# Kernel optimization log

Measured on AMD Instinct MI355X. Metric: run time of the kernel, lower is better.

The kernel has to match this reference:

```python
import jax, jax.numpy as jnp
import numpy as np

EPS = 1e-5  # BatchNorm eps (torch default)
PAD = 1
K = 9  # 3x3 kernel points

def conv3x3(x, w, b):
    # x: [B,C,H,W], w: [O,C,3,3]
    y = jax.lax.conv_general_dilated(x, w, (1, 1), ((PAD, PAD), (PAD, PAD)),
                                     dimension_numbers=('NCHW', 'OIHW', 'NCHW'))
    return y + b[None, :, None, None]

def deform_conv2d(x, offset, mask, weight, bias):
    # Modulated deformable conv v2, stride 1, pad 1, 3x3 kernel.
    # x: [B,C,H,W]; offset: [B,2K,H,W] (first K = dy, last K = dx); mask: [B,K,H,W]
    B, C, H, W = x.shape
    ki, kj = jnp.meshgrid(jnp.arange(3), jnp.arange(3), indexing='ij')
    ki = ki.reshape(K).astype(x.dtype)
    kj = kj.reshape(K).astype(x.dtype)
    dy = offset[:, :K].transpose(0, 2, 3, 1)   # [B,H,W,K]
    dx = offset[:, K:].transpose(0, 2, 3, 1)
    m = mask.transpose(0, 2, 3, 1)             # [B,H,W,K]
    hs = jnp.arange(H, dtype=x.dtype)
    ws = jnp.arange(W, dtype=x.dtype)
    py = hs[None, :, None, None] - PAD + ki[None, None, None, :] + dy  # [B,H,W,K]
    px = ws[None, None, :, None] - PAD + kj[None, None, None, :] + dx
    y0 = jnp.floor(py)
    x0 = jnp.floor(px)
    wy1 = py - y0
    wx1 = px - x0
    wy0 = 1.0 - wy1
    wx0 = 1.0 - wx1

    def gather(yi, xi):
        valid = ((yi >= 0) & (yi < H) & (xi >= 0) & (xi < W)).astype(x.dtype)
        yc = jnp.clip(yi, 0, H - 1).astype(jnp.int32)
        xc = jnp.clip(xi, 0, W - 1).astype(jnp.int32)
        g = jax.vmap(lambda img, yb, xb: img[:, yb, xb])(x, yc, xc)  # [B,C,H,W,K]
        return g * valid[:, None]

    val = (gather(y0, x0) * (wy0 * wx0)[:, None]
           + gather(y0, x0 + 1.0) * (wy0 * wx1)[:, None]
           + gather(y0 + 1.0, x0) * (wy1 * wx0)[:, None]
           + gather(y0 + 1.0, x0 + 1.0) * (wy1 * wx1)[:, None])
    val = val * m[:, None]  # modulation
    out = jnp.einsum('bchwk,ock->bohw', val, weight.reshape(weight.shape[0], C, K))
    return out + bias[None, :, None, None]

def dcnv2(x, w_om, b_om, w, b, gamma, beta, mean, var):
    om = conv3x3(x, w_om, b_om)               # [B,27,H,W]
    o1, o2, mr = jnp.split(om, 3, axis=1)
    offset = jnp.concatenate([o1, o2], axis=1)  # [B,18,H,W]
    mask = jax.nn.sigmoid(mr)
    y = deform_conv2d(x, offset, mask, w, b)
    scale = (gamma / jnp.sqrt(var + EPS))[None, :, None, None]
    y = (y - mean[None, :, None, None]) * scale + beta[None, :, None, None]
    return jax.nn.silu(y)

def setup_inputs() -> dict:
    key = jax.random.key(0)
    ks = jax.random.split(key, 9)
    B, C, H, W = 4, 256, 128, 128
    C4 = C // 4
    return {
        'x': jax.random.normal(ks[0], (B, C, H, W), jnp.float32),
        'w': jax.random.normal(ks[1], (4, C4, C4, 3, 3), jnp.float32) * 0.05,
        'b': jax.random.normal(ks[2], (4, C4), jnp.float32) * 0.05,
        'w_om': jax.random.normal(ks[3], (4, 27, C4, 3, 3), jnp.float32) * 0.01,
        'b_om': jax.random.normal(ks[4], (4, 27), jnp.float32) * 0.01,
        'gamma': jax.random.normal(ks[5], (4, C4), jnp.float32) * 0.1 + 1.0,
        'beta': jax.random.normal(ks[6], (4, C4), jnp.float32) * 0.1,
        'mean': jax.random.normal(ks[7], (4, C4), jnp.float32) * 0.1,
        'var': jax.random.uniform(ks[8], (4, C4), jnp.float32, minval=0.5, maxval=1.5),
    }

def reference(x, w, b, w_om, b_om, gamma, beta, mean, var):
    B, C, H, W = x.shape
    C4 = C // 4
    # channel-split into 4 independent groups, vmap identical DCNv2 over groups
    xg = x.reshape(B, 4, C4, H, W).transpose(1, 0, 2, 3, 4)  # [4,B,C4,H,W]
    yg = jax.vmap(dcnv2)(xg, w_om, b_om, w, b, gamma, beta, mean, var)
    return yg.transpose(1, 0, 2, 3, 4).reshape(B, C, H, W)
```

## Files before the change

### kernel.cpp

```cpp
#include <hip/hip_runtime.h>
#include <math.h>

#define Hs 128
#define Ws 128
#define HWs 16384

typedef __attribute__((ext_vector_type(8))) short short8;
typedef __attribute__((ext_vector_type(8))) __bf16 bf16x8;
typedef __attribute__((ext_vector_type(4))) float f32x4;

static __device__ __forceinline__ float bf2f(unsigned short u) {
    union { unsigned int i; float f; } v; v.i = ((unsigned int)u) << 16; return v.f;
}
static __device__ __forceinline__ unsigned short f2bf(float f) {
    unsigned int u = __builtin_bit_cast(unsigned int, f);
    return (unsigned short)((u + 0x7fffu + ((u >> 16) & 1u)) >> 16);
}
static __device__ __forceinline__ unsigned int pack2bf(float a0, float a1) {
    return (unsigned int)f2bf(a0) | ((unsigned int)f2bf(a1) << 16);
}
static __device__ __forceinline__ f32x4 mfma16(short8 a, short8 b, f32x4 c) {
    return __builtin_amdgcn_mfma_f32_16x16x32_bf16(
        __builtin_bit_cast(bf16x8, a), __builtin_bit_cast(bf16x8, b), c, 0, 0, 0);
}

__global__ void k_prep(const float* __restrict__ w, const float* __restrict__ b,
                       const float* __restrict__ w_om,
                       const float* __restrict__ gamma, const float* __restrict__ beta,
                       const float* __restrict__ mean, const float* __restrict__ var,
                       unsigned short* __restrict__ w2, unsigned short* __restrict__ wom2,
                       float* __restrict__ scsh) {
    int idx = blockIdx.x * 256 + threadIdx.x;
    if (idx < 4 * 64 * 576) {
        int go = idx / 576;
        int ck = idx - go * 576;
        int k = ck >> 6, c = ck & 63;
        w2[idx] = f2bf(w[go * 576 + c * 9 + k]);
    }
    if (idx < 4 * 32 * 576) {
        int gj = idx / 576;
        int g = gj >> 5, j = gj & 31;
        int ck = idx - gj * 576;
        int k = ck >> 6, c = ck & 63;
        float v = (j < 27) ? w_om[(g * 27 + j) * 576 + c * 9 + k] : 0.f;
        wom2[idx] = f2bf(v);
    }
    if (idx < 256) {
        float sc = gamma[idx] * rsqrtf(var[idx] + 1e-5f);
        scsh[idx] = sc;
        scsh[256 + idx] = (b[idx] - mean[idx]) * sc + beta[idx];
    }
}

__global__ __launch_bounds__(256) void k_xt(const float* __restrict__ x,
                                            unsigned short* __restrict__ xT) {
    const int img = blockIdx.y;
    const int g = img >> 2, bb = img & 3;
    const int p0 = blockIdx.x * 64;
    const int tid = threadIdx.x;
    __shared__ float t[64 * 65];

    const float* xg = x + (size_t)(bb * 256 + g * 64) * HWs + p0;
    const int pr = tid & 63, cw = tid >> 6;
#pragma unroll
    for (int i = 0; i < 16; ++i) {
        int c = i * 4 + cw;
        t[c * 65 + pr] = xg[(size_t)c * HWs + pr];
    }
    __syncthreads();
    const int p = tid >> 2, c16 = (tid & 3) * 16;
    unsigned short* dst = xT + (size_t)img * HWs * 64 + (size_t)(p0 + p) * 64 + c16;
    unsigned int rr[8];
#pragma unroll
    for (int q = 0; q < 8; ++q)
        rr[q] = pack2bf(t[(c16 + 2 * q) * 65 + p], t[(c16 + 2 * q + 1) * 65 + p]);
    *(uint4*)dst       = make_uint4(rr[0], rr[1], rr[2], rr[3]);
    *(uint4*)(dst + 8) = make_uint4(rr[4], rr[5], rr[6], rr[7]);
}

__global__ __launch_bounds__(256, 2) void k_off(const unsigned short* __restrict__ xT,
                                                const unsigned short* __restrict__ wom2,
                                                const float* __restrict__ b_om,
                                                float* __restrict__ om) {
    const int img = blockIdx.y;
    const int g = img >> 2;
    const int h = blockIdx.x;
    const int tid = threadIdx.x;
    const int lane = tid & 63, wv = tid >> 6;
    const int mt = wv & 1, nh = wv >> 1;
    const int m = lane & 15, q = lane >> 4;

    __shared__ unsigned short xrow[3 * 130 * 72];

    const unsigned short* xTi = xT + (size_t)img * HWs * 64;
    for (int i = tid; i < 3 * 130 * 8; i += 256) {
        int rr = i / 1040;
        int rem = i - rr * 1040;
        int px = rem >> 3, j = rem & 7;
        int gh = h + rr - 1, gw = px - 1;
        uint4 v = make_uint4(0, 0, 0, 0);
        if (gh >= 0 && gh < Hs && gw >= 0 && gw < Ws)
            v = *(const uint4*)(xTi + (size_t)(gh * Ws + gw) * 64 + j * 8);
        *(uint4*)&xrow[(rr * 130 + px) * 72 + j * 8] = v;
    }

    short8 afrag[18];
    const unsigned short* wb = wom2 + (size_t)(g * 32 + mt * 16 + m) * 576 + q * 8;
#pragma unroll
    for (int t = 0; t < 18; ++t) afrag[t] = *(const short8*)(wb + t * 32);

    f32x4 acc[4];
#pragma unroll
    for (int t = 0; t < 4; ++t) acc[t] = (f32x4){0.f, 0.f, 0.f, 0.f};

    __syncthreads();

#pragma unroll
    for (int k = 0; k < 9; ++k) {
        const int ki = k / 3, kj = k - ki * 3;
#pragma unroll
        for (int s = 0; s < 2; ++s) {
#pragma unroll
            for (int t = 0; t < 4; ++t) {
                int px = (nh * 4 + t) * 16 + m + kj;
                short8 bfrag = *(const short8*)&xrow[(ki * 130 + px) * 72 + (s * 4 + q) * 8];
                acc[t] = mfma16(afrag[k * 2 + s], bfrag, acc[t]);
            }
        }
    }

    float* omi = om + (size_t)img * 27 * HWs + h * Ws;
#pragma unroll
    for (int t = 0; t < 4; ++t) {
#pragma unroll
        for (int r = 0; r < 4; ++r) {
            int j = mt * 16 + q * 4 + r;
            if (j < 27) {
                float v = acc[t][r] + b_om[g * 27 + j];
                if (j >= 18) v = 1.f / (1.f + __expf(-v));
                omi[(size_t)j * HWs + (nh * 4 + t) * 16 + m] = v;
            }
        }
    }
}

__global__ __launch_bounds__(256, 3) void k_def(const unsigned short* __restrict__ xT,
                                                const float* __restrict__ om,
                                                const unsigned short* __restrict__ w2,
                                                const float* __restrict__ scsh,
                                                float* __restrict__ out) {
    const int img = blockIdx.y;
    const int g = img >> 2, bb = img & 3;
    const int p0 = blockIdx.x * 64;
    const int tid = threadIdx.x;
    const int lane = tid & 63, wv = tid >> 6;
    const int m = lane & 15, q = lane >> 4;

    __shared__ int   pO[4][576];
    __shared__ float pW[4][576];
    __shared__ unsigned short val[64 * 72];
    __shared__ float lsc[64], lsh[64];

    if (tid < 64) {
        lsc[tid] = scsh[g * 64 + tid];
        lsh[tid] = scsh[256 + g * 64 + tid];
    }

    const float* omg = om + (size_t)img * 27 * HWs;
    for (int idx = tid; idx < 576; idx += 256) {
        int k = idx >> 6, pp = idx & 63;
        int p = p0 + pp;
        int h = p >> 7, w = p & 127;
        float dy = omg[k * HWs + p];
        float dx = omg[(9 + k) * HWs + p];
        float mk = omg[(18 + k) * HWs + p];
        int ki = k / 3, kj = k - ki * 3;
        float py = (float)(h - 1 + ki) + dy;
        float px = (float)(w - 1 + kj) + dx;
        float fy = floorf(py), fx = floorf(px);
        float wy1 = py - fy, wx1 = px - fx;
        float wy0 = 1.f - wy1, wx0 = 1.f - wx1;
        int y0 = (int)fy, x0 = (int)fx, y1 = y0 + 1, x1 = x0 + 1;
        bool vy0 = (y0 >= 0) && (y0 < Hs), vy1 = (y1 >= 0) && (y1 < Hs);
        bool vx0 = (x0 >= 0) && (x0 < Ws), vx1 = (x1 >= 0) && (x1 < Ws);
        int cy0 = min(max(y0, 0), Hs - 1), cy1 = min(max(y1, 0), Hs - 1);
        int cx0 = min(max(x0, 0), Ws - 1), cx1 = min(max(x1, 0), Ws - 1);
        pO[0][idx] = cy0 * Ws + cx0;
        pO[1][idx] = cy0 * Ws + cx1;
        pO[2][idx] = cy1 * Ws + cx0;
        pO[3][idx] = cy1 * Ws + cx1;
        pW[0][idx] = (vy0 && vx0) ? wy0 * wx0 * mk : 0.f;
        pW[1][idx] = (vy0 && vx1) ? wy0 * wx1 * mk : 0.f;
        pW[2][idx] = (vy1 && vx0) ? wy1 * wx0 * mk : 0.f;
        pW[3][idx] = (vy1 && vx1) ? wy1 * wx1 * mk : 0.f;
    }

    short8 afrag[18];
    const unsigned short* wb = w2 + (size_t)(g * 64 + wv * 16 + m) * 576 + q * 8;
#pragma unroll
    for (int t = 0; t < 18; ++t) afrag[t] = *(const short8*)(wb + t * 32);

    f32x4 acc[4];
#pragma unroll
    for (int t = 0; t < 4; ++t) acc[t] = (f32x4){0.f, 0.f, 0.f, 0.f};

    const unsigned short* xTi = xT + (size_t)img * HWs * 64;
    const int p = tid >> 2, c4 = tid & 3;

#pragma unroll
    for (int k = 0; k < 9; ++k) {
        __syncthreads();
        const int kb = k * 64 + p;
        const int off0 = pO[0][kb], off1 = pO[1][kb], off2 = pO[2][kb], off3 = pO[3][kb];
        const float w0f = pW[0][kb], w1f = pW[1][kb], w2f = pW[2][kb], w3f = pW[3][kb];
        const unsigned short* s0 = xTi + (size_t)off0 * 64;
        const unsigned short* s1 = xTi + (size_t)off1 * 64;
        const unsigned short* s2 = xTi + (size_t)off2 * 64;
        const unsigned short* s3 = xTi + (size_t)off3 * 64;
#pragma unroll
        for (int it = 0; it < 2; ++it) {
            const int oc8 = (c4 + it * 4) * 8;
            short8 x0v = *(const short8*)(s0 + oc8);
            short8 x1v = *(const short8*)(s1 + oc8);
            short8 x2v = *(const short8*)(s2 + oc8);
            short8 x3v = *(const short8*)(s3 + oc8);
            unsigned int rr[4];
#pragma unroll
            for (int e = 0; e < 4; ++e) {
                float a0 = w0f * bf2f((unsigned short)x0v[2 * e])
                         + w1f * bf2f((unsigned short)x1v[2 * e])
                         + w2f * bf2f((unsigned short)x2v[2 * e])
                         + w3f * bf2f((unsigned short)x3v[2 * e]);
                float a1 = w0f * bf2f((unsigned short)x0v[2 * e + 1])
                         + w1f * bf2f((unsigned short)x1v[2 * e + 1])
                         + w2f * bf2f((unsigned short)x2v[2 * e + 1])
                         + w3f * bf2f((unsigned short)x3v[2 * e + 1]);
                rr[e] = pack2bf(a0, a1);
            }
            *(uint4*)&val[p * 72 + oc8] = make_uint4(rr[0], rr[1], rr[2], rr[3]);
        }
        __syncthreads();
#pragma unroll
        for (int s = 0; s < 2; ++s) {
#pragma unroll
            for (int t = 0; t < 4; ++t) {
                short8 bfrag = *(const short8*)&val[(t * 16 + m) * 72 + s * 32 + q * 8];
                acc[t] = mfma16(afrag[k * 2 + s], bfrag, acc[t]);
            }
        }
    }

    float* outg = out + ((size_t)bb * 256 + g * 64) * HWs + p0;
#pragma unroll
    for (int t = 0; t < 4; ++t) {
#pragma unroll
        for (int r = 0; r < 4; ++r) {
            int o = wv * 16 + q * 4 + r;
            float y = acc[t][r] * lsc[o] + lsh[o];
            outg[(size_t)o * HWs + t * 16 + m] = y / (1.f + __expf(-y));
        }
    }
}

extern "C" void kernel_launch(void* const* d_in, const int* in_sizes, int n_in,
                              void* d_out, int out_size, void* d_ws, size_t ws_size,
                              hipStream_t stream) {
    const float* x     = (const float*)d_in[0];
    const float* w     = (const float*)d_in[1];
    const float* b     = (const float*)d_in[2];
    const float* w_om  = (const float*)d_in[3];
    const float* b_om  = (const float*)d_in[4];
    const float* gamma = (const float*)d_in[5];
    const float* beta  = (const float*)d_in[6];
    const float* mean  = (const float*)d_in[7];
    const float* var   = (const float*)d_in[8];
    float* out = (float*)d_out;

    char* ws = (char*)d_ws;
    float* om            = (float*)ws;
    unsigned short* xT   = (unsigned short*)(ws + 28311552);
    unsigned short* w2   = (unsigned short*)(ws + 61865984);
    unsigned short* wom2 = (unsigned short*)(ws + 62160896);
    float* scsh          = (float*)(ws + 62308352);

    hipLaunchKernelGGL(k_prep, dim3(576), dim3(256), 0, stream,
                       w, b, w_om, gamma, beta, mean, var, w2, wom2, scsh);
    hipLaunchKernelGGL(k_xt, dim3(256, 16), dim3(256), 0, stream, x, xT);
    hipLaunchKernelGGL(k_off, dim3(128, 16), dim3(256), 0, stream, xT, wom2, b_om, om);
    hipLaunchKernelGGL(k_def, dim3(256, 16), dim3(256), 0, stream, xT, om, w2, scsh, out);
}
```

Measured before the change: 296.2 us.

## Double-buffer deformable gather and fold weight prep into transpose kernel

```diff
diff --git a/kernel.cpp b/kernel.cpp
--- a/kernel.cpp
+++ b/kernel.cpp
@@ -24,40 +24,46 @@
         __builtin_bit_cast(bf16x8, a), __builtin_bit_cast(bf16x8, b), c, 0, 0, 0);
 }
 
-__global__ void k_prep(const float* __restrict__ w, const float* __restrict__ b,
-                       const float* __restrict__ w_om,
-                       const float* __restrict__ gamma, const float* __restrict__ beta,
-                       const float* __restrict__ mean, const float* __restrict__ var,
-                       unsigned short* __restrict__ w2, unsigned short* __restrict__ wom2,
-                       float* __restrict__ scsh) {
-    int idx = blockIdx.x * 256 + threadIdx.x;
-    if (idx < 4 * 64 * 576) {
-        int go = idx / 576;
-        int ck = idx - go * 576;
-        int k = ck >> 6, c = ck & 63;
-        w2[idx] = f2bf(w[go * 576 + c * 9 + k]);
-    }
-    if (idx < 4 * 32 * 576) {
-        int gj = idx / 576;
-        int g = gj >> 5, j = gj & 31;
-        int ck = idx - gj * 576;
-        int k = ck >> 6, c = ck & 63;
-        float v = (j < 27) ? w_om[(g * 27 + j) * 576 + c * 9 + k] : 0.f;
-        wom2[idx] = f2bf(v);
-    }
-    if (idx < 256) {
-        float sc = gamma[idx] * rsqrtf(var[idx] + 1e-5f);
-        scsh[idx] = sc;
-        scsh[256 + idx] = (b[idx] - mean[idx]) * sc + beta[idx];
-    }
-}
-
 __global__ __launch_bounds__(256) void k_xt(const float* __restrict__ x,
-                                            unsigned short* __restrict__ xT) {
+                                            const float* __restrict__ w,
+                                            const float* __restrict__ b,
+                                            const float* __restrict__ w_om,
+                                            const float* __restrict__ gamma,
+                                            const float* __restrict__ beta,
+                                            const float* __restrict__ mean,
+                                            const float* __restrict__ var,
+                                            unsigned short* __restrict__ xT,
+                                            unsigned short* __restrict__ w2,
+                                            unsigned short* __restrict__ wom2,
+                                            float* __restrict__ scsh) {
+    const int tid = threadIdx.x;
+    const int flatb = blockIdx.y * 256 + blockIdx.x;
+    if (flatb < 576) {
+        int idx = flatb * 256 + tid;
+        if (idx < 4 * 64 * 576) {
+            int go = idx / 576;
+            int ck = idx - go * 576;
+            int k = ck >> 6, c = ck & 63;
+            w2[idx] = f2bf(w[go * 576 + c * 9 + k]);
+        }
+        if (idx < 4 * 32 * 576) {
+            int gj = idx / 576;
+            int g = gj >> 5, j = gj & 31;
+            int ck = idx - gj * 576;
+            int k = ck >> 6, c = ck & 63;
+            float v = (j < 27) ? w_om[(g * 27 + j) * 576 + c * 9 + k] : 0.f;
+            wom2[idx] = f2bf(v);
+        }
+        if (idx < 256) {
+            float sc = gamma[idx] * rsqrtf(var[idx] + 1e-5f);
+            scsh[idx] = sc;
+            scsh[256 + idx] = (b[idx] - mean[idx]) * sc + beta[idx];
+        }
+    }
+
     const int img = blockIdx.y;
     const int g = img >> 2, bb = img & 3;
     const int p0 = blockIdx.x * 64;
-    const int tid = threadIdx.x;
     __shared__ float t[64 * 65];
 
     const float* xg = x + (size_t)(bb * 256 + g * 64) * HWs + p0;
@@ -158,7 +164,7 @@
 
     __shared__ int   pO[4][576];
     __shared__ float pW[4][576];
-    __shared__ unsigned short val[64 * 72];
+    __shared__ unsigned short val[2][64 * 72];
     __shared__ float lsc[64], lsh[64];
 
     if (tid < 64) {
@@ -207,44 +213,62 @@
     const unsigned short* xTi = xT + (size_t)img * HWs * 64;
     const int p = tid >> 2, c4 = tid & 3;
 
-#pragma unroll
-    for (int k = 0; k < 9; ++k) {
-        __syncthreads();
+    __syncthreads();
+
+    uint4 gth[8];
+    float wf0, wf1, wf2, wf3;
+    auto fetch = [&](int k) {
         const int kb = k * 64 + p;
         const int off0 = pO[0][kb], off1 = pO[1][kb], off2 = pO[2][kb], off3 = pO[3][kb];
-        const float w0f = pW[0][kb], w1f = pW[1][kb], w2f = pW[2][kb], w3f = pW[3][kb];
+        wf0 = pW[0][kb]; wf1 = pW[1][kb]; wf2 = pW[2][kb]; wf3 = pW[3][kb];
         const unsigned short* s0 = xTi + (size_t)off0 * 64;
         const unsigned short* s1 = xTi + (size_t)off1 * 64;
         const unsigned short* s2 = xTi + (size_t)off2 * 64;
         const unsigned short* s3 = xTi + (size_t)off3 * 64;
+        gth[0] = *(const uint4*)(s0 + c4 * 8);
+        gth[1] = *(const uint4*)(s1 + c4 * 8);
+        gth[2] = *(const uint4*)(s2 + c4 * 8);
+        gth[3] = *(const uint4*)(s3 + c4 * 8);
+        gth[4] = *(const uint4*)(s0 + (c4 + 4) * 8);
+        gth[5] = *(const uint4*)(s1 + (c4 + 4) * 8);
+        gth[6] = *(const uint4*)(s2 + (c4 + 4) * 8);
+        gth[7] = *(const uint4*)(s3 + (c4 + 4) * 8);
+    };
+    fetch(0);
+
+#pragma unroll
+    for (int k = 0; k < 9; ++k) {
+        unsigned short* vb = &val[k & 1][0];
 #pragma unroll
         for (int it = 0; it < 2; ++it) {
             const int oc8 = (c4 + it * 4) * 8;
-            short8 x0v = *(const short8*)(s0 + oc8);
-            short8 x1v = *(const short8*)(s1 + oc8);
-            short8 x2v = *(const short8*)(s2 + oc8);
-            short8 x3v = *(const short8*)(s3 + oc8);
             unsigned int rr[4];
 #pragma unroll
             for (int e = 0; e < 4; ++e) {
-                float a0 = w0f * bf2f((unsigned short)x0v[2 * e])
-                         + w1f * bf2f((unsigned short)x1v[2 * e])
-                         + w2f * bf2f((unsigned short)x2v[2 * e])
-                         + w3f * bf2f((unsigned short)x3v[2 * e]);
-                float a1 = w0f * bf2f((unsigned short)x0v[2 * e + 1])
-                         + w1f * bf2f((unsigned short)x1v[2 * e + 1])
-                         + w2f * bf2f((unsigned short)x2v[2 * e + 1])
-                         + w3f * bf2f((unsigned short)x3v[2 * e + 1]);
+                const unsigned int u0 = ((const unsigned int*)&gth[it * 4 + 0])[e];
+                const unsigned int u1 = ((const unsigned int*)&gth[it * 4 + 1])[e];
+                const unsigned int u2 = ((const unsigned int*)&gth[it * 4 + 2])[e];
+                const unsigned int u3 = ((const unsigned int*)&gth[it * 4 + 3])[e];
+                float a0 = wf0 * bf2f((unsigned short)(u0 & 0xffff))
+                         + wf1 * bf2f((unsigned short)(u1 & 0xffff))
+                         + wf2 * bf2f((unsigned short)(u2 & 0xffff))
+                         + wf3 * bf2f((unsigned short)(u3 & 0xffff));
+                float a1 = wf0 * bf2f((unsigned short)(u0 >> 16))
+                         + wf1 * bf2f((unsigned short)(u1 >> 16))
+                         + wf2 * bf2f((unsigned short)(u2 >> 16))
+                         + wf3 * bf2f((unsigned short)(u3 >> 16));
                 rr[e] = pack2bf(a0, a1);
             }
-            *(uint4*)&val[p * 72 + oc8] = make_uint4(rr[0], rr[1], rr[2], rr[3]);
-        }
+            *(uint4*)&vb[p * 72 + oc8] = make_uint4(rr[0], rr[1], rr[2], rr[3]);
+        }
+        if (k < 8) fetch(k + 1);
         __syncthreads();
+        const unsigned short* vr = &val[k & 1][0];
 #pragma unroll
         for (int s = 0; s < 2; ++s) {
 #pragma unroll
             for (int t = 0; t < 4; ++t) {
-                short8 bfrag = *(const short8*)&val[(t * 16 + m) * 72 + s * 32 + q * 8];
+                short8 bfrag = *(const short8*)&vr[(t * 16 + m) * 72 + s * 32 + q * 8];
                 acc[t] = mfma16(afrag[k * 2 + s], bfrag, acc[t]);
             }
         }
@@ -283,9 +307,8 @@
     unsigned short* wom2 = (unsigned short*)(ws + 62160896);
     float* scsh          = (float*)(ws + 62308352);
 
-    hipLaunchKernelGGL(k_prep, dim3(576), dim3(256), 0, stream,
-                       w, b, w_om, gamma, beta, mean, var, w2, wom2, scsh);
-    hipLaunchKernelGGL(k_xt, dim3(256, 16), dim3(256), 0, stream, x, xT);
+    hipLaunchKernelGGL(k_xt, dim3(256, 16), dim3(256), 0, stream,
+                       x, w, b, w_om, gamma, beta, mean, var, xT, w2, wom2, scsh);
     hipLaunchKernelGGL(k_off, dim3(128, 16), dim3(256), 0, stream, xT, wom2, b_om, om);
     hipLaunchKernelGGL(k_def, dim3(256, 16), dim3(256), 0, stream, xT, om, w2, scsh, out);
 }
```

Result: faster. 269.7 us (-8.9%).
